# Kernel optimization log

Hardware: AMD Instinct MI355X
Metric: run time of the kernel (lower is better)

Reference implementation:

```python
import jax, jax.numpy as jnp
import numpy as np

N_NODES = 100000
N_EDGES = 600000
NFEAT = 128
HIDDEN = 64
NCLASS = 40


def _sage_conv(x, edge_index, Wl, bl, Wr):
    """PyG SAGEConv with mean aggregation.

    out = lin_l(mean_{j in N(i)} x_j) + lin_r(x_i)
    edge_index[0] = source j, edge_index[1] = target i.
    """
    src, dst = edge_index[0], edge_index[1]
    n = x.shape[0]
    # scatter-mean: sum messages then divide by in-degree (0-degree -> 0)
    msg_sum = jax.ops.segment_sum(x[src], dst, num_segments=n)          # [N, F]
    deg = jax.ops.segment_sum(jnp.ones_like(src, dtype=x.dtype), dst,
                              num_segments=n)                            # [N]
    agg = msg_sum / jnp.maximum(deg, 1.0)[:, None]
    return agg @ Wl + bl + x @ Wr


def setup_inputs() -> dict:
    key = jax.random.key(0)
    ks = jax.random.split(key, 8)
    x = jax.random.normal(ks[0], (N_NODES, NFEAT), dtype=jnp.float32)
    edge_index = jax.random.randint(ks[1], (2, N_EDGES), 0, N_NODES, dtype=jnp.int64)
    s1 = 1.0 / np.sqrt(NFEAT)
    s2 = 1.0 / np.sqrt(HIDDEN)
    return {
        "x": x,
        "edge_index": edge_index,
        "W1l": jax.random.uniform(ks[2], (NFEAT, HIDDEN), jnp.float32, -s1, s1),
        "b1": jnp.zeros((HIDDEN,), jnp.float32),
        "W1r": jax.random.uniform(ks[3], (NFEAT, HIDDEN), jnp.float32, -s1, s1),
        "W2l": jax.random.uniform(ks[4], (HIDDEN, NCLASS), jnp.float32, -s2, s2),
        "b2": jnp.zeros((NCLASS,), jnp.float32),
        "W2r": jax.random.uniform(ks[5], (HIDDEN, NCLASS), jnp.float32, -s2, s2),
    }


def reference(x, edge_index, W1l, b1, W1r, W2l, b2, W2r):
    h = _sage_conv(x, edge_index, W1l, b1, W1r)   # [N, 64]
    h = jax.nn.sigmoid(h)
    out = _sage_conv(h, edge_index, W2l, b2, W2r)  # [N, nclass]
    return out
```

## Files before the change

kernel.cpp:

```cpp
#include <hip/hip_runtime.h>
#include <hip/hip_bf16.h>


#define N_FEAT 128
#define HID 64
#define NCLS 40
#define NE_BLK 2048

typedef short short8 __attribute__((ext_vector_type(8)));
typedef float floatx4 __attribute__((ext_vector_type(4)));

static __device__ __forceinline__ short f2bf(float x) {
    __hip_bfloat16 h = __float2bfloat16(x);
    return __builtin_bit_cast(short, h);
}
static __device__ __forceinline__ float bf2f(unsigned short u) {
    unsigned int v = ((unsigned int)u) << 16;
    return __builtin_bit_cast(float, v);
}

__global__ void prep_hist(const float* __restrict__ W1l, const float* __restrict__ W1r,
                          const float* __restrict__ W2l, const float* __restrict__ W2r,
                          unsigned short* __restrict__ wt1,
                          unsigned short* __restrict__ wt2,
                          int* __restrict__ flags,
                          const int* __restrict__ ei, int ne, int n,
                          int* __restrict__ bh, int nbe) {
    __shared__ int bins[512];
    const int b = blockIdx.x, t = threadIdx.x;
    const int nbuck = (n + 255) >> 8;
    for (int i = t; i < nbuck; i += 256) bins[i] = 0;
    __syncthreads();
    const int e0 = b * NE_BLK;
    const int lim = (e0 + NE_BLK < ne) ? (e0 + NE_BLK) : ne;
    for (int e = e0 + t; e < lim; e += 256)
        atomicAdd(&bins[ei[ne + e] >> 8], 1);

    int i = b * 256 + t;
    if (i < 128 * 128) {
        int nn = i >> 7, k = i & 127;
        float v = (nn < 64) ? W1l[k * 64 + nn] : W1r[k * 64 + (nn - 64)];
        wt1[nn * 128 + k] = (unsigned short)f2bf(v);
    } else if (i < 128 * 128 + 48 * 128) {
        int j = i - 128 * 128;
        int nn = j >> 7, k = j & 127;
        float v = 0.f;
        if (nn < 40)
            v = (k < 64) ? W2l[k * 40 + nn] : W2r[(k - 64) * 40 + nn];
        wt2[nn * 128 + k] = (unsigned short)f2bf(v);
    }
    if (i < 256) flags[i] = 0;

    __syncthreads();
    for (int j = t; j < nbuck; j += 256) bh[j * nbe + b] = bins[j];
}

__global__ void scan_fused(const int* __restrict__ in, int* __restrict__ pre,
                           int m, int* __restrict__ bsums,
                           int* __restrict__ flags) {
    __shared__ int lds[256];
    __shared__ int look[128];
    __shared__ int sprefix;
    const int b = blockIdx.x, t = threadIdx.x;
    const int base = b * 2048 + t * 8;
    int v[8], s = 0;
#pragma unroll
    for (int i = 0; i < 8; ++i) {
        int idx = base + i;
        v[i] = (idx < m) ? in[idx] : 0;
        s += v[i];
    }
    lds[t] = s;
    __syncthreads();
    for (int o = 1; o < 256; o <<= 1) {
        int y = (t >= o) ? lds[t - o] : 0;
        __syncthreads();
        lds[t] += y;
        __syncthreads();
    }
    if (t == 255) {
        __hip_atomic_store(&bsums[b], lds[255], __ATOMIC_RELEASE,
                           __HIP_MEMORY_SCOPE_AGENT);
        __hip_atomic_store(&flags[b], 1, __ATOMIC_RELEASE,
                           __HIP_MEMORY_SCOPE_AGENT);
    }
    if (t < 128) look[t] = 0;
    __syncthreads();
    if (t < b) {
        while (__hip_atomic_load(&flags[t], __ATOMIC_ACQUIRE,
                                 __HIP_MEMORY_SCOPE_AGENT) == 0) {}
        look[t] = __hip_atomic_load(&bsums[t], __ATOMIC_RELAXED,
                                    __HIP_MEMORY_SCOPE_AGENT);
    }
    __syncthreads();
    if (t == 0) {
        int p = 0;
        for (int i = 0; i < b; ++i) p += look[i];
        sprefix = p;
    }
    __syncthreads();
    int run = ((t == 0) ? 0 : lds[t - 1]) + sprefix;
#pragma unroll
    for (int i = 0; i < 8; ++i) {
        run += v[i];
        int idx = base + i;
        if (idx < m) pre[idx + 1] = run;
    }
    if (b == 0 && t == 0) pre[0] = 0;
}

__global__ void bucket_scatter(const int* __restrict__ ei, int ne, int n,
                               const int* __restrict__ sbase,
                               int* __restrict__ ebuf, int nbe) {
    __shared__ int bins[512];
    const int b = blockIdx.x, t = threadIdx.x;
    const int nbuck = (n + 255) >> 8;
    for (int i = t; i < nbuck; i += 256) bins[i] = 0;
    __syncthreads();
    const int e0 = b * NE_BLK;
    const int lim = (e0 + NE_BLK < ne) ? (e0 + NE_BLK) : ne;
    for (int e = e0 + t; e < lim; e += 256) {
        int d = ei[ne + e];
        int s = ei[e];
        int bk = d >> 8;
        int r = atomicAdd(&bins[bk], 1);
        int p = sbase[bk * nbe + b] + r;
        ebuf[p] = (int)(((unsigned)(d & 255) << 24) | (unsigned)s);
    }
}

__global__ void bucket_build(const int* __restrict__ ebuf,
                             const int* __restrict__ sbase, int nbe, int n,
                             int ne, int* __restrict__ off,
                             int* __restrict__ csr) {
    __shared__ int cnt[256];
    __shared__ int sc[256];
    __shared__ int pos[256];
    const int b = blockIdx.x;
    const int t = threadIdx.x;
    const int nbuck = (n + 255) >> 8;
    const int s0 = sbase[b * nbe];
    const int s1 = (b + 1 < nbuck) ? sbase[(b + 1) * nbe] : ne;
    cnt[t] = 0;
    __syncthreads();
    for (int i = s0 + t; i < s1; i += 256)
        atomicAdd(&cnt[((unsigned)ebuf[i]) >> 24], 1);
    __syncthreads();
    int v = cnt[t];
    sc[t] = v;
    __syncthreads();
    for (int o = 1; o < 256; o <<= 1) {
        int y = (t >= o) ? sc[t - o] : 0;
        __syncthreads();
        sc[t] += y;
        __syncthreads();
    }
    int g = b * 256 + t;
    if (g < n) off[g + 1] = s0 + sc[t];
    if (b == 0 && t == 0) off[0] = 0;
    pos[t] = s0 + sc[t] - v;
    __syncthreads();
    for (int i = s0 + t; i < s1; i += 256) {
        unsigned w = (unsigned)ebuf[i];
        int p = atomicAdd(&pos[w >> 24], 1);
        csr[p] = (int)(w & 0xFFFFFFu);
    }
}

template <int K, int MH, bool AF32>
__global__ __launch_bounds__(256) void gemm_mfma(
    const void* __restrict__ Ain, const unsigned short* __restrict__ Wt,
    unsigned short* __restrict__ Zl, unsigned short* __restrict__ Zr, int n) {
    constexpr int M = 2 * MH;
    constexpr int LDA = K + 8;
    constexpr int MT = (M + 15) / 16;
    constexpr int KS = K / 32;
    constexpr int QROW = K / 8;
    __shared__ __align__(16) short At[64 * LDA];
    __shared__ __align__(16) short Bt[M * LDA];

    const int t = threadIdx.x;
    const int nodeBase = blockIdx.x * 64;

    for (int q = t; q < 64 * QROW; q += 256) {
        int row = q / QROW;
        int k0 = (q % QROW) * 8;
        int node = nodeBase + row;
        short8 s = {0, 0, 0, 0, 0, 0, 0, 0};
        if (node < n) {
            if (AF32) {
                const float* A = (const float*)Ain + (size_t)node * K + k0;
                float4 v0 = *(const float4*)A;
                float4 v1 = *(const float4*)(A + 4);
                s[0] = f2bf(v0.x); s[1] = f2bf(v0.y);
                s[2] = f2bf(v0.z); s[3] = f2bf(v0.w);
                s[4] = f2bf(v1.x); s[5] = f2bf(v1.y);
                s[6] = f2bf(v1.z); s[7] = f2bf(v1.w);
            } else {
                s = *(const short8*)((const short*)Ain + (size_t)node * K + k0);
            }
        }
        *(short8*)&At[row * LDA + k0] = s;
    }
    for (int q = t; q < M * QROW; q += 256) {
        int row = q / QROW;
        int k0 = (q % QROW) * 8;
        *(short8*)&Bt[row * LDA + k0] =
            *(const short8*)((const short*)Wt + (size_t)row * K + k0);
    }
    __syncthreads();

    const int wave = t >> 6;
    const int lane = t & 63;
    const int m0 = wave * 16;
    const int fl = lane & 15;
    const int quad = lane >> 4;

    floatx4 acc[MT];
#pragma unroll
    for (int nt = 0; nt < MT; ++nt) acc[nt] = (floatx4){0.f, 0.f, 0.f, 0.f};

#pragma unroll
    for (int ks = 0; ks < KS; ++ks) {
        const int kb = ks * 32 + quad * 8;
        short8 a = *(const short8*)&At[(m0 + fl) * LDA + kb];
#pragma unroll
        for (int nt = 0; nt < MT; ++nt) {
            short8 b = *(const short8*)&Bt[(nt * 16 + fl) * LDA + kb];
            acc[nt] = __builtin_amdgcn_mfma_f32_16x16x32_bf16(a, b, acc[nt], 0, 0, 0);
        }
    }

#pragma unroll
    for (int nt = 0; nt < MT; ++nt) {
        const int col = nt * 16 + fl;
#pragma unroll
        for (int r = 0; r < 4; ++r) {
            int node = nodeBase + m0 + quad * 4 + r;
            if (node < n) {
                unsigned short v = (unsigned short)f2bf(acc[nt][r]);
                if (col < MH)
                    Zl[(size_t)node * MH + col] = v;
                else
                    Zr[(size_t)node * MH + (col - MH)] = v;
            }
        }
    }
}

__global__ __launch_bounds__(256) void gemm2cat(
    const unsigned short* __restrict__ aggh, const unsigned short* __restrict__ h,
    const unsigned short* __restrict__ Wt, const float* __restrict__ bias,
    float* __restrict__ out, int n) {
    constexpr int K = 128;
    constexpr int LDA = K + 8;
    constexpr int M = 48;
    constexpr int MT = 3;
    __shared__ __align__(16) short At[64 * LDA];
    __shared__ __align__(16) short Bt[M * LDA];

    const int t = threadIdx.x;
    const int nodeBase = blockIdx.x * 64;

    for (int q = t; q < 64 * 16; q += 256) {
        int row = q >> 4;
        int k0 = (q & 15) * 8;
        int node = nodeBase + row;
        short8 s = {0, 0, 0, 0, 0, 0, 0, 0};
        if (node < n) {
            const unsigned short* src =
                (k0 < 64) ? (aggh + (size_t)node * 64 + k0)
                          : (h + (size_t)node * 64 + (k0 - 64));
            s = *(const short8*)src;
        }
        *(short8*)&At[row * LDA + k0] = s;
    }
    for (int q = t; q < M * 16; q += 256) {
        int row = q >> 4;
        int k0 = (q & 15) * 8;
        *(short8*)&Bt[row * LDA + k0] =
            *(const short8*)((const short*)Wt + (size_t)row * K + k0);
    }
    __syncthreads();

    const int wave = t >> 6;
    const int lane = t & 63;
    const int m0 = wave * 16;
    const int fl = lane & 15;
    const int quad = lane >> 4;

    floatx4 acc[MT];
#pragma unroll
    for (int nt = 0; nt < MT; ++nt) acc[nt] = (floatx4){0.f, 0.f, 0.f, 0.f};

#pragma unroll
    for (int ks = 0; ks < 4; ++ks) {
        const int kb = ks * 32 + quad * 8;
        short8 a = *(const short8*)&At[(m0 + fl) * LDA + kb];
#pragma unroll
        for (int nt = 0; nt < MT; ++nt) {
            short8 b = *(const short8*)&Bt[(nt * 16 + fl) * LDA + kb];
            acc[nt] = __builtin_amdgcn_mfma_f32_16x16x32_bf16(a, b, acc[nt], 0, 0, 0);
        }
    }

#pragma unroll
    for (int nt = 0; nt < MT; ++nt) {
        const int col = nt * 16 + fl;
        if (col < NCLS) {
            float bv = bias[col];
#pragma unroll
            for (int r = 0; r < 4; ++r) {
                int node = nodeBase + m0 + quad * 4 + r;
                if (node < n)
                    out[(size_t)node * NCLS + col] = acc[nt][r] + bv;
            }
        }
    }
}

template <int MODE>
__global__ void agg64_kernel(const unsigned short* __restrict__ Zl,
                             const unsigned short* __restrict__ Zr,
                             const int* __restrict__ off,
                             const int* __restrict__ csr,
                             const float* __restrict__ bias,
                             unsigned short* __restrict__ out, int n) {
    const int wid = blockIdx.x * (blockDim.x >> 6) + (threadIdx.x >> 6);
    const int node0 = wid * 2;
    if (node0 >= n) return;
    const int lane = threadIdx.x & 63;
    const int g = lane >> 3;
    const int c = lane & 7;

    const bool has1 = (node0 + 1) < n;
    const int s0 = off[node0];
    const int e0 = off[node0 + 1];
    const int e1 = has1 ? off[node0 + 2] : e0;
    const int d0 = e0 - s0;
    const int d1 = e1 - e0;

    int ed0 = (d0 > 0) ? csr[s0 + ((lane < d0) ? lane : (d0 - 1))] : 0;
    int ed1 = (d1 > 0) ? csr[e0 + ((lane < d1) ? lane : (d1 - 1))] : 0;

    float a0[8], a1[8];
#pragma unroll
    for (int j = 0; j < 8; ++j) { a0[j] = 0.f; a1[j] = 0.f; }

    const int dm = (d0 > d1) ? d0 : d1;
    for (int e = 0; e < dm; e += 8) {
        const int r = e + g;
        int i0, i1;
        if (e < 64) {
            i0 = __shfl(ed0, (r < d0) ? r : ((d0 > 0) ? d0 - 1 : 0));
            i1 = __shfl(ed1, (r < d1) ? r : ((d1 > 0) ? d1 - 1 : 0));
        } else {
            i0 = (d0 > 0) ? csr[s0 + ((r < d0) ? r : d0 - 1)] : 0;
            i1 = (d1 > 0) ? csr[e0 + ((r < d1) ? r : d1 - 1)] : 0;
        }
        const float w0 = (r < d0) ? 1.f : 0.f;
        const float w1 = (r < d1) ? 1.f : 0.f;
        uint4 v0 = *(const uint4*)(Zl + (size_t)i0 * 64 + c * 8);
        uint4 v1 = *(const uint4*)(Zl + (size_t)i1 * 64 + c * 8);
        a0[0] = fmaf(w0, bf2f((unsigned short)(v0.x & 0xffffu)), a0[0]);
        a0[1] = fmaf(w0, bf2f((unsigned short)(v0.x >> 16)), a0[1]);
        a0[2] = fmaf(w0, bf2f((unsigned short)(v0.y & 0xffffu)), a0[2]);
        a0[3] = fmaf(w0, bf2f((unsigned short)(v0.y >> 16)), a0[3]);
        a0[4] = fmaf(w0, bf2f((unsigned short)(v0.z & 0xffffu)), a0[4]);
        a0[5] = fmaf(w0, bf2f((unsigned short)(v0.z >> 16)), a0[5]);
        a0[6] = fmaf(w0, bf2f((unsigned short)(v0.w & 0xffffu)), a0[6]);
        a0[7] = fmaf(w0, bf2f((unsigned short)(v0.w >> 16)), a0[7]);
        a1[0] = fmaf(w1, bf2f((unsigned short)(v1.x & 0xffffu)), a1[0]);
        a1[1] = fmaf(w1, bf2f((unsigned short)(v1.x >> 16)), a1[1]);
        a1[2] = fmaf(w1, bf2f((unsigned short)(v1.y & 0xffffu)), a1[2]);
        a1[3] = fmaf(w1, bf2f((unsigned short)(v1.y >> 16)), a1[3]);
        a1[4] = fmaf(w1, bf2f((unsigned short)(v1.z & 0xffffu)), a1[4]);
        a1[5] = fmaf(w1, bf2f((unsigned short)(v1.z >> 16)), a1[5]);
        a1[6] = fmaf(w1, bf2f((unsigned short)(v1.w & 0xffffu)), a1[6]);
        a1[7] = fmaf(w1, bf2f((unsigned short)(v1.w >> 16)), a1[7]);
    }
#pragma unroll
    for (int o = 8; o < 64; o <<= 1) {
#pragma unroll
        for (int j = 0; j < 8; ++j) {
            a0[j] += __shfl_xor(a0[j], o);
            a1[j] += __shfl_xor(a1[j], o);
        }
    }
    if (g < 2) {
        const int node = node0 + g;
        if (node < n) {
            const int dd = g ? d1 : d0;
            float rr[8];
#pragma unroll
            for (int j = 0; j < 8; ++j) rr[j] = g ? a1[j] : a0[j];
            const float inv = 1.0f / fmaxf((float)dd, 1.0f);
            float r0, r1, r2, r3, r4, r5, r6, r7;
            if (MODE == 0) {
                uint4 z = *(const uint4*)(Zr + (size_t)node * 64 + c * 8);
                float4 b0 = ((const float4*)bias)[c * 2];
                float4 b1 = ((const float4*)bias)[c * 2 + 1];
                r0 = rr[0] * inv + bf2f((unsigned short)(z.x & 0xffffu)) + b0.x;
                r1 = rr[1] * inv + bf2f((unsigned short)(z.x >> 16)) + b0.y;
                r2 = rr[2] * inv + bf2f((unsigned short)(z.y & 0xffffu)) + b0.z;
                r3 = rr[3] * inv + bf2f((unsigned short)(z.y >> 16)) + b0.w;
                r4 = rr[4] * inv + bf2f((unsigned short)(z.z & 0xffffu)) + b1.x;
                r5 = rr[5] * inv + bf2f((unsigned short)(z.z >> 16)) + b1.y;
                r6 = rr[6] * inv + bf2f((unsigned short)(z.w & 0xffffu)) + b1.z;
                r7 = rr[7] * inv + bf2f((unsigned short)(z.w >> 16)) + b1.w;
                r0 = 1.0f / (1.0f + __expf(-r0));
                r1 = 1.0f / (1.0f + __expf(-r1));
                r2 = 1.0f / (1.0f + __expf(-r2));
                r3 = 1.0f / (1.0f + __expf(-r3));
                r4 = 1.0f / (1.0f + __expf(-r4));
                r5 = 1.0f / (1.0f + __expf(-r5));
                r6 = 1.0f / (1.0f + __expf(-r6));
                r7 = 1.0f / (1.0f + __expf(-r7));
            } else {
                r0 = rr[0] * inv; r1 = rr[1] * inv;
                r2 = rr[2] * inv; r3 = rr[3] * inv;
                r4 = rr[4] * inv; r5 = rr[5] * inv;
                r6 = rr[6] * inv; r7 = rr[7] * inv;
            }
            uint4 p;
            p.x = (unsigned int)(unsigned short)f2bf(r0) |
                  ((unsigned int)(unsigned short)f2bf(r1) << 16);
            p.y = (unsigned int)(unsigned short)f2bf(r2) |
                  ((unsigned int)(unsigned short)f2bf(r3) << 16);
            p.z = (unsigned int)(unsigned short)f2bf(r4) |
                  ((unsigned int)(unsigned short)f2bf(r5) << 16);
            p.w = (unsigned int)(unsigned short)f2bf(r6) |
                  ((unsigned int)(unsigned short)f2bf(r7) << 16);
            *(uint4*)(out + (size_t)node * 64 + c * 8) = p;
        }
    }
}

extern "C" void kernel_launch(void* const* d_in, const int* in_sizes, int n_in,
                              void* d_out, int out_size, void* d_ws,
                              size_t ws_size, hipStream_t stream) {
    const float* x = (const float*)d_in[0];
    const int* ei = (const int*)d_in[1];
    const float* W1l = (const float*)d_in[2];
    const float* b1 = (const float*)d_in[3];
    const float* W1r = (const float*)d_in[4];
    const float* W2l = (const float*)d_in[5];
    const float* b2 = (const float*)d_in[6];
    const float* W2r = (const float*)d_in[7];
    float* out = (float*)d_out;

    const int n = in_sizes[0] / N_FEAT;
    const int ne = in_sizes[1] / 2;

    const int nbe = (ne + NE_BLK - 1) / NE_BLK;
    const int nbuck = (n + 255) >> 8;
    const int tot = nbuck * nbe;

    unsigned short* zl1 = (unsigned short*)d_ws;
    unsigned short* zr1 = zl1 + (size_t)n * HID;
    unsigned short* h = zr1 + (size_t)n * HID;
    unsigned short* aggh = h + (size_t)n * HID;
    unsigned short* wt1 = aggh + (size_t)n * HID;
    unsigned short* wt2 = wt1 + 128 * 128;
    int* off = (int*)(wt2 + 48 * 128);
    int* csr = off + (n + 1);
    int* ebuf = csr + ne;
    int* bh = ebuf + ne;
    int* sbase = bh + tot;
    int* bsums = sbase + (tot + 1);
    int* flags = bsums + 256;

    const int gblocks = (n + 63) / 64;
    const int ablocks = (n + 7) / 8;
    const int nsb = (tot + 2047) / 2048;

    prep_hist<<<nbe, 256, 0, stream>>>(W1l, W1r, W2l, W2r, wt1, wt2, flags,
                                       ei, ne, n, bh, nbe);
    gemm_mfma<N_FEAT, HID, true><<<gblocks, 256, 0, stream>>>(x, wt1, zl1, zr1, n);
    scan_fused<<<nsb, 256, 0, stream>>>(bh, sbase, tot, bsums, flags);
    bucket_scatter<<<nbe, 256, 0, stream>>>(ei, ne, n, sbase, ebuf, nbe);
    bucket_build<<<nbuck, 256, 0, stream>>>(ebuf, sbase, nbe, n, ne, off, csr);
    agg64_kernel<0><<<ablocks, 256, 0, stream>>>(zl1, zr1, off, csr, b1, h, n);
    agg64_kernel<1><<<ablocks, 256, 0, stream>>>(h, nullptr, off, csr, nullptr,
                                                 aggh, n);
    gemm2cat<<<gblocks, 256, 0, stream>>>(aggh, h, wt2, b2, out, n);
}
```

Before: 218.0 us.

## Fuse layer-2 aggregation into GEMM2 and merge bucket scatter with GEMM1

Layer-2 mean aggregation now writes straight into the shared-memory A tile of the second GEMM, so the intermediate aggregated buffer and its global round trip are gone. The bucket scatter and the first GEMM run as one launch that splits work by block index, which removes a kernel launch and lets the two independent jobs overlap. Aggregation now processes 64 nodes per block and stages the block's CSR neighbour list in shared memory, falling back to global reads when it exceeds ECAP. In exchange the larger shared-memory footprint may lower occupancy, and blocks with very different node degrees may be unevenly loaded.

After: 216.6 us. Within noise of the previous version (-0.6%).

```diff
diff --git a/kernel.cpp b/kernel.cpp
--- a/kernel.cpp
+++ b/kernel.cpp
@@ -6,6 +6,7 @@
 #define HID 64
 #define NCLS 40
 #define NE_BLK 2048
+#define ECAP 1536
 
 typedef short short8 __attribute__((ext_vector_type(8)));
 typedef float floatx4 __attribute__((ext_vector_type(4)));
@@ -17,6 +18,16 @@
 static __device__ __forceinline__ float bf2f(unsigned short u) {
     unsigned int v = ((unsigned int)u) << 16;
     return __builtin_bit_cast(float, v);
+}
+static __device__ __forceinline__ void acc8(float* a, uint4 v, float w) {
+    a[0] = fmaf(w, bf2f((unsigned short)(v.x & 0xffffu)), a[0]);
+    a[1] = fmaf(w, bf2f((unsigned short)(v.x >> 16)), a[1]);
+    a[2] = fmaf(w, bf2f((unsigned short)(v.y & 0xffffu)), a[2]);
+    a[3] = fmaf(w, bf2f((unsigned short)(v.y >> 16)), a[3]);
+    a[4] = fmaf(w, bf2f((unsigned short)(v.z & 0xffffu)), a[4]);
+    a[5] = fmaf(w, bf2f((unsigned short)(v.z >> 16)), a[5]);
+    a[6] = fmaf(w, bf2f((unsigned short)(v.w & 0xffffu)), a[6]);
+    a[7] = fmaf(w, bf2f((unsigned short)(v.w >> 16)), a[7]);
 }
 
 __global__ void prep_hist(const float* __restrict__ W1l, const float* __restrict__ W1r,
@@ -109,23 +120,103 @@
     if (b == 0 && t == 0) pre[0] = 0;
 }
 
-__global__ void bucket_scatter(const int* __restrict__ ei, int ne, int n,
-                               const int* __restrict__ sbase,
-                               int* __restrict__ ebuf, int nbe) {
-    __shared__ int bins[512];
-    const int b = blockIdx.x, t = threadIdx.x;
-    const int nbuck = (n + 255) >> 8;
-    for (int i = t; i < nbuck; i += 256) bins[i] = 0;
-    __syncthreads();
-    const int e0 = b * NE_BLK;
-    const int lim = (e0 + NE_BLK < ne) ? (e0 + NE_BLK) : ne;
-    for (int e = e0 + t; e < lim; e += 256) {
-        int d = ei[ne + e];
-        int s = ei[e];
-        int bk = d >> 8;
-        int r = atomicAdd(&bins[bk], 1);
-        int p = sbase[bk * nbe + b] + r;
-        ebuf[p] = (int)(((unsigned)(d & 255) << 24) | (unsigned)s);
+static __device__ __forceinline__ void gemm1_body(
+    short* __restrict__ smem, const float* __restrict__ x,
+    const unsigned short* __restrict__ Wt, unsigned short* __restrict__ Zl,
+    unsigned short* __restrict__ Zr, int n, int bid) {
+    constexpr int K = 128, LDA = K + 8, M = 128, MT = 8, KS = 4, QROW = 16;
+    short* At = smem;
+    short* Bt = smem + 64 * LDA;
+    const int t = threadIdx.x;
+    const int nodeBase = bid * 64;
+
+    for (int q = t; q < 64 * QROW; q += 256) {
+        int row = q / QROW;
+        int k0 = (q % QROW) * 8;
+        int node = nodeBase + row;
+        short8 s = {0, 0, 0, 0, 0, 0, 0, 0};
+        if (node < n) {
+            const float* A = x + (size_t)node * K + k0;
+            float4 v0 = *(const float4*)A;
+            float4 v1 = *(const float4*)(A + 4);
+            s[0] = f2bf(v0.x); s[1] = f2bf(v0.y);
+            s[2] = f2bf(v0.z); s[3] = f2bf(v0.w);
+            s[4] = f2bf(v1.x); s[5] = f2bf(v1.y);
+            s[6] = f2bf(v1.z); s[7] = f2bf(v1.w);
+        }
+        *(short8*)&At[row * LDA + k0] = s;
+    }
+    for (int q = t; q < M * QROW; q += 256) {
+        int row = q / QROW;
+        int k0 = (q % QROW) * 8;
+        *(short8*)&Bt[row * LDA + k0] =
+            *(const short8*)((const short*)Wt + (size_t)row * K + k0);
+    }
+    __syncthreads();
+
+    const int wave = t >> 6;
+    const int lane = t & 63;
+    const int m0 = wave * 16;
+    const int fl = lane & 15;
+    const int quad = lane >> 4;
+
+    floatx4 acc[MT];
+#pragma unroll
+    for (int nt = 0; nt < MT; ++nt) acc[nt] = (floatx4){0.f, 0.f, 0.f, 0.f};
+
+#pragma unroll
+    for (int ks = 0; ks < KS; ++ks) {
+        const int kb = ks * 32 + quad * 8;
+        short8 a = *(const short8*)&At[(m0 + fl) * LDA + kb];
+#pragma unroll
+        for (int nt = 0; nt < MT; ++nt) {
+            short8 b = *(const short8*)&Bt[(nt * 16 + fl) * LDA + kb];
+            acc[nt] = __builtin_amdgcn_mfma_f32_16x16x32_bf16(a, b, acc[nt], 0, 0, 0);
+        }
+    }
+
+#pragma unroll
+    for (int nt = 0; nt < MT; ++nt) {
+        const int col = nt * 16 + fl;
+#pragma unroll
+        for (int r = 0; r < 4; ++r) {
+            int node = nodeBase + m0 + quad * 4 + r;
+            if (node < n) {
+                unsigned short v = (unsigned short)f2bf(acc[nt][r]);
+                if (col < HID)
+                    Zl[(size_t)node * HID + col] = v;
+                else
+                    Zr[(size_t)node * HID + (col - HID)] = v;
+            }
+        }
+    }
+}
+
+__global__ __launch_bounds__(256) void scatter_gemm1(
+    const int* __restrict__ ei, int ne, int n, const int* __restrict__ sbase,
+    int* __restrict__ ebuf, int nbe, const float* __restrict__ x,
+    const unsigned short* __restrict__ wt1, unsigned short* __restrict__ zl,
+    unsigned short* __restrict__ zr) {
+    __shared__ __align__(16) short smem[(64 + 128) * 136];
+    const int b = blockIdx.x;
+    if (b < nbe) {
+        int* bins = (int*)smem;
+        const int t = threadIdx.x;
+        const int nbuck = (n + 255) >> 8;
+        for (int i = t; i < nbuck; i += 256) bins[i] = 0;
+        __syncthreads();
+        const int e0 = b * NE_BLK;
+        const int lim = (e0 + NE_BLK < ne) ? (e0 + NE_BLK) : ne;
+        for (int e = e0 + t; e < lim; e += 256) {
+            int d = ei[ne + e];
+            int s = ei[e];
+            int bk = d >> 8;
+            int r = atomicAdd(&bins[bk], 1);
+            int p = sbase[bk * nbe + b] + r;
+            ebuf[p] = (int)(((unsigned)(d & 255) << 24) | (unsigned)s);
+        }
+    } else {
+        gemm1_body(smem, x, wt1, zl, zr, n, b - nbe);
     }
 }
 
@@ -167,271 +258,200 @@
     }
 }
 
-template <int K, int MH, bool AF32>
-__global__ __launch_bounds__(256) void gemm_mfma(
-    const void* __restrict__ Ain, const unsigned short* __restrict__ Wt,
-    unsigned short* __restrict__ Zl, unsigned short* __restrict__ Zr, int n) {
-    constexpr int M = 2 * MH;
-    constexpr int LDA = K + 8;
-    constexpr int MT = (M + 15) / 16;
-    constexpr int KS = K / 32;
-    constexpr int QROW = K / 8;
+__global__ __launch_bounds__(256) void agg_h(
+    const unsigned short* __restrict__ Zl, const unsigned short* __restrict__ Zr,
+    const int* __restrict__ off, const int* __restrict__ csr,
+    const float* __restrict__ bias, unsigned short* __restrict__ hout, int n) {
+    __shared__ int offs[65];
+    __shared__ int elist[ECAP];
+    const int t = threadIdx.x;
+    const int base = blockIdx.x * 64;
+    if (t < 65) {
+        int idx = base + t;
+        offs[t] = off[(idx <= n) ? idx : n];
+    }
+    __syncthreads();
+    const int E0 = offs[0];
+    const int nedge = offs[64] - E0;
+    const bool direct = (nedge > ECAP);
+    if (!direct)
+        for (int j = t; j < nedge; j += 256) elist[j] = csr[E0 + j];
+    __syncthreads();
+
+    const int lane = t & 63;
+    const int wave = t >> 6;
+    const int g = lane >> 3, c = lane & 7;
+
+    for (int p = 0; p < 8; ++p) {
+        const int i0 = wave * 16 + 2 * p, i1 = i0 + 1;
+        const int s0 = offs[i0] - E0, d0 = offs[i0 + 1] - offs[i0];
+        const int s1 = offs[i1] - E0, d1 = offs[i1 + 1] - offs[i1];
+        float a0[8], a1[8];
+#pragma unroll
+        for (int j = 0; j < 8; ++j) { a0[j] = 0.f; a1[j] = 0.f; }
+        const int dm = (d0 > d1) ? d0 : d1;
+        for (int r0 = 0; r0 < dm; r0 += 8) {
+            const int r = r0 + g;
+            int sl0 = s0 + ((r < d0) ? r : ((d0 > 0) ? d0 - 1 : 0));
+            int sl1 = s1 + ((r < d1) ? r : ((d1 > 0) ? d1 - 1 : 0));
+            int j0 = (d0 > 0) ? (direct ? csr[E0 + sl0] : elist[sl0]) : 0;
+            int j1 = (d1 > 0) ? (direct ? csr[E0 + sl1] : elist[sl1]) : 0;
+            uint4 v0 = *(const uint4*)(Zl + (size_t)j0 * 64 + c * 8);
+            uint4 v1 = *(const uint4*)(Zl + (size_t)j1 * 64 + c * 8);
+            acc8(a0, v0, (r < d0) ? 1.f : 0.f);
+            acc8(a1, v1, (r < d1) ? 1.f : 0.f);
+        }
+#pragma unroll
+        for (int o = 8; o < 64; o <<= 1) {
+#pragma unroll
+            for (int j = 0; j < 8; ++j) {
+                a0[j] += __shfl_xor(a0[j], o);
+                a1[j] += __shfl_xor(a1[j], o);
+            }
+        }
+        if (g < 2) {
+            const int i = g ? i1 : i0;
+            const int node = base + i;
+            if (node < n) {
+                const int dd = g ? d1 : d0;
+                const float inv = 1.0f / fmaxf((float)dd, 1.0f);
+                float rr[8];
+#pragma unroll
+                for (int j = 0; j < 8; ++j) rr[j] = (g ? a1[j] : a0[j]) * inv;
+                uint4 z = *(const uint4*)(Zr + (size_t)node * 64 + c * 8);
+                float4 b0 = ((const float4*)bias)[c * 2];
+                float4 b1 = ((const float4*)bias)[c * 2 + 1];
+                rr[0] += bf2f((unsigned short)(z.x & 0xffffu)) + b0.x;
+                rr[1] += bf2f((unsigned short)(z.x >> 16)) + b0.y;
+                rr[2] += bf2f((unsigned short)(z.y & 0xffffu)) + b0.z;
+                rr[3] += bf2f((unsigned short)(z.y >> 16)) + b0.w;
+                rr[4] += bf2f((unsigned short)(z.z & 0xffffu)) + b1.x;
+                rr[5] += bf2f((unsigned short)(z.z >> 16)) + b1.y;
+                rr[6] += bf2f((unsigned short)(z.w & 0xffffu)) + b1.z;
+                rr[7] += bf2f((unsigned short)(z.w >> 16)) + b1.w;
+#pragma unroll
+                for (int j = 0; j < 8; ++j)
+                    rr[j] = 1.0f / (1.0f + __expf(-rr[j]));
+                uint4 pk;
+                pk.x = (unsigned int)(unsigned short)f2bf(rr[0]) |
+                       ((unsigned int)(unsigned short)f2bf(rr[1]) << 16);
+                pk.y = (unsigned int)(unsigned short)f2bf(rr[2]) |
+                       ((unsigned int)(unsigned short)f2bf(rr[3]) << 16);
+                pk.z = (unsigned int)(unsigned short)f2bf(rr[4]) |
+                       ((unsigned int)(unsigned short)f2bf(rr[5]) << 16);
+                pk.w = (unsigned int)(unsigned short)f2bf(rr[6]) |
+                       ((unsigned int)(unsigned short)f2bf(rr[7]) << 16);
+                *(uint4*)(hout + (size_t)node * 64 + c * 8) = pk;
+            }
+        }
+    }
+}
+
+__global__ __launch_bounds__(256) void agg_gemm2(
+    const unsigned short* __restrict__ h, const unsigned short* __restrict__ Wt,
+    const float* __restrict__ bias, const int* __restrict__ off,
+    const int* __restrict__ csr, float* __restrict__ out, int n) {
+    constexpr int LDA = 136;
     __shared__ __align__(16) short At[64 * LDA];
-    __shared__ __align__(16) short Bt[M * LDA];
-
+    __shared__ __align__(16) short Bt[48 * LDA];
+    __shared__ int offs[65];
+    __shared__ int elist[ECAP];
     const int t = threadIdx.x;
-    const int nodeBase = blockIdx.x * 64;
-
-    for (int q = t; q < 64 * QROW; q += 256) {
-        int row = q / QROW;
-        int k0 = (q % QROW) * 8;
-        int node = nodeBase + row;
+    const int base = blockIdx.x * 64;
+    if (t < 65) {
+        int idx = base + t;
+        offs[t] = off[(idx <= n) ? idx : n];
+    }
+    __syncthreads();
+    const int E0 = offs[0];
+    const int nedge = offs[64] - E0;
+    const bool direct = (nedge > ECAP);
+    if (!direct)
+        for (int j = t; j < nedge; j += 256) elist[j] = csr[E0 + j];
+    for (int q = t; q < 64 * 8; q += 256) {
+        int row = q >> 3, k0 = (q & 7) * 8;
+        int node = base + row;
         short8 s = {0, 0, 0, 0, 0, 0, 0, 0};
-        if (node < n) {
-            if (AF32) {
-                const float* A = (const float*)Ain + (size_t)node * K + k0;
-                float4 v0 = *(const float4*)A;
-                float4 v1 = *(const float4*)(A + 4);
-                s[0] = f2bf(v0.x); s[1] = f2bf(v0.y);
-                s[2] = f2bf(v0.z); s[3] = f2bf(v0.w);
-                s[4] = f2bf(v1.x); s[5] = f2bf(v1.y);
-                s[6] = f2bf(v1.z); s[7] = f2bf(v1.w);
-            } else {
-                s = *(const short8*)((const short*)Ain + (size_t)node * K + k0);
+        if (node < n) s = *(const short8*)(h + (size_t)node * 64 + k0);
+        *(short8*)&At[row * LDA + 64 + k0] = s;
+    }
+    for (int q = t; q < 48 * 16; q += 256) {
+        int row = q >> 4, k0 = (q & 15) * 8;
+        *(short8*)&Bt[row * LDA + k0] =
+            *(const short8*)((const short*)Wt + (size_t)row * 128 + k0);
+    }
+    __syncthreads();
+
+    const int lane = t & 63;
+    const int wave = t >> 6;
+    const int g = lane >> 3, c = lane & 7;
+    for (int p = 0; p < 8; ++p) {
+        const int i0 = wave * 16 + 2 * p, i1 = i0 + 1;
+        const int s0 = offs[i0] - E0, d0 = offs[i0 + 1] - offs[i0];
+        const int s1 = offs[i1] - E0, d1 = offs[i1 + 1] - offs[i1];
+        float a0[8], a1[8];
+#pragma unroll
+        for (int j = 0; j < 8; ++j) { a0[j] = 0.f; a1[j] = 0.f; }
+        const int dm = (d0 > d1) ? d0 : d1;
+        for (int r0 = 0; r0 < dm; r0 += 8) {
+            const int r = r0 + g;
+            int sl0 = s0 + ((r < d0) ? r : ((d0 > 0) ? d0 - 1 : 0));
+            int sl1 = s1 + ((r < d1) ? r : ((d1 > 0) ? d1 - 1 : 0));
+            int j0 = (d0 > 0) ? (direct ? csr[E0 + sl0] : elist[sl0]) : 0;
+            int j1 = (d1 > 0) ? (direct ? csr[E0 + sl1] : elist[sl1]) : 0;
+            uint4 v0 = *(const uint4*)(h + (size_t)j0 * 64 + c * 8);
+            uint4 v1 = *(const uint4*)(h + (size_t)j1 * 64 + c * 8);
+            acc8(a0, v0, (r < d0) ? 1.f : 0.f);
+            acc8(a1, v1, (r < d1) ? 1.f : 0.f);
+        }
+#pragma unroll
+        for (int o = 8; o < 64; o <<= 1) {
+#pragma unroll
+            for (int j = 0; j < 8; ++j) {
+                a0[j] += __shfl_xor(a0[j], o);
+                a1[j] += __shfl_xor(a1[j], o);
             }
         }
-        *(short8*)&At[row * LDA + k0] = s;
-    }
-    for (int q = t; q < M * QROW; q += 256) {
-        int row = q / QROW;
-        int k0 = (q % QROW) * 8;
-        *(short8*)&Bt[row * LDA + k0] =
-            *(const short8*)((const short*)Wt + (size_t)row * K + k0);
-    }
-    __syncthreads();
-
-    const int wave = t >> 6;
-    const int lane = t & 63;
+        if (g < 2) {
+            const int i = g ? i1 : i0;
+            const int dd = g ? d1 : d0;
+            const float inv = 1.0f / fmaxf((float)dd, 1.0f);
+            short8 s;
+#pragma unroll
+            for (int j = 0; j < 8; ++j)
+                s[j] = f2bf((g ? a1[j] : a0[j]) * inv);
+            *(short8*)&At[i * LDA + c * 8] = s;
+        }
+    }
+    __syncthreads();
+
     const int m0 = wave * 16;
     const int fl = lane & 15;
     const int quad = lane >> 4;
-
-    floatx4 acc[MT];
-#pragma unroll
-    for (int nt = 0; nt < MT; ++nt) acc[nt] = (floatx4){0.f, 0.f, 0.f, 0.f};
-
-#pragma unroll
-    for (int ks = 0; ks < KS; ++ks) {
-        const int kb = ks * 32 + quad * 8;
-        short8 a = *(const short8*)&At[(m0 + fl) * LDA + kb];
-#pragma unroll
-        for (int nt = 0; nt < MT; ++nt) {
-            short8 b = *(const short8*)&Bt[(nt * 16 + fl) * LDA + kb];
-            acc[nt] = __builtin_amdgcn_mfma_f32_16x16x32_bf16(a, b, acc[nt], 0, 0, 0);
-        }
-    }
-
-#pragma unroll
-    for (int nt = 0; nt < MT; ++nt) {
-        const int col = nt * 16 + fl;
-#pragma unroll
-        for (int r = 0; r < 4; ++r) {
-            int node = nodeBase + m0 + quad * 4 + r;
-            if (node < n) {
-                unsigned short v = (unsigned short)f2bf(acc[nt][r]);
-                if (col < MH)
-                    Zl[(size_t)node * MH + col] = v;
-                else
-                    Zr[(size_t)node * MH + (col - MH)] = v;
-            }
-        }
-    }
-}
-
-__global__ __launch_bounds__(256) void gemm2cat(
-    const unsigned short* __restrict__ aggh, const unsigned short* __restrict__ h,
-    const unsigned short* __restrict__ Wt, const float* __restrict__ bias,
-    float* __restrict__ out, int n) {
-    constexpr int K = 128;
-    constexpr int LDA = K + 8;
-    constexpr int M = 48;
-    constexpr int MT = 3;
-    __shared__ __align__(16) short At[64 * LDA];
-    __shared__ __align__(16) short Bt[M * LDA];
-
-    const int t = threadIdx.x;
-    const int nodeBase = blockIdx.x * 64;
-
-    for (int q = t; q < 64 * 16; q += 256) {
-        int row = q >> 4;
-        int k0 = (q & 15) * 8;
-        int node = nodeBase + row;
-        short8 s = {0, 0, 0, 0, 0, 0, 0, 0};
-        if (node < n) {
-            const unsigned short* src =
-                (k0 < 64) ? (aggh + (size_t)node * 64 + k0)
-                          : (h + (size_t)node * 64 + (k0 - 64));
-            s = *(const short8*)src;
-        }
-        *(short8*)&At[row * LDA + k0] = s;
-    }
-    for (int q = t; q < M * 16; q += 256) {
-        int row = q >> 4;
-        int k0 = (q & 15) * 8;
-        *(short8*)&Bt[row * LDA + k0] =
-            *(const short8*)((const short*)Wt + (size_t)row * K + k0);
-    }
-    __syncthreads();
-
-    const int wave = t >> 6;
-    const int lane = t & 63;
-    const int m0 = wave * 16;
-    const int fl = lane & 15;
-    const int quad = lane >> 4;
-
-    floatx4 acc[MT];
-#pragma unroll
-    for (int nt = 0; nt < MT; ++nt) acc[nt] = (floatx4){0.f, 0.f, 0.f, 0.f};
-
+    floatx4 acc[3];
+#pragma unroll
+    for (int nt = 0; nt < 3; ++nt) acc[nt] = (floatx4){0.f, 0.f, 0.f, 0.f};
 #pragma unroll
     for (int ks = 0; ks < 4; ++ks) {
         const int kb = ks * 32 + quad * 8;
         short8 a = *(const short8*)&At[(m0 + fl) * LDA + kb];
 #pragma unroll
-        for (int nt = 0; nt < MT; ++nt) {
+        for (int nt = 0; nt < 3; ++nt) {
             short8 b = *(const short8*)&Bt[(nt * 16 + fl) * LDA + kb];
             acc[nt] = __builtin_amdgcn_mfma_f32_16x16x32_bf16(a, b, acc[nt], 0, 0, 0);
         }
     }
-
-#pragma unroll
-    for (int nt = 0; nt < MT; ++nt) {
+#pragma unroll
+    for (int nt = 0; nt < 3; ++nt) {
         const int col = nt * 16 + fl;
         if (col < NCLS) {
             float bv = bias[col];
 #pragma unroll
             for (int r = 0; r < 4; ++r) {
-                int node = nodeBase + m0 + quad * 4 + r;
+                int node = base + m0 + quad * 4 + r;
                 if (node < n)
                     out[(size_t)node * NCLS + col] = acc[nt][r] + bv;
             }
-        }
-    }
-}
-
-template <int MODE>
-__global__ void agg64_kernel(const unsigned short* __restrict__ Zl,
-                             const unsigned short* __restrict__ Zr,
-                             const int* __restrict__ off,
-                             const int* __restrict__ csr,
-                             const float* __restrict__ bias,
-                             unsigned short* __restrict__ out, int n) {
-    const int wid = blockIdx.x * (blockDim.x >> 6) + (threadIdx.x >> 6);
-    const int node0 = wid * 2;
-    if (node0 >= n) return;
-    const int lane = threadIdx.x & 63;
-    const int g = lane >> 3;
-    const int c = lane & 7;
-
-    const bool has1 = (node0 + 1) < n;
-    const int s0 = off[node0];
-    const int e0 = off[node0 + 1];
-    const int e1 = has1 ? off[node0 + 2] : e0;
-    const int d0 = e0 - s0;
-    const int d1 = e1 - e0;
-
-    int ed0 = (d0 > 0) ? csr[s0 + ((lane < d0) ? lane : (d0 - 1))] : 0;
-    int ed1 = (d1 > 0) ? csr[e0 + ((lane < d1) ? lane : (d1 - 1))] : 0;
-
-    float a0[8], a1[8];
-#pragma unroll
-    for (int j = 0; j < 8; ++j) { a0[j] = 0.f; a1[j] = 0.f; }
-
-    const int dm = (d0 > d1) ? d0 : d1;
-    for (int e = 0; e < dm; e += 8) {
-        const int r = e + g;
-        int i0, i1;
-        if (e < 64) {
-            i0 = __shfl(ed0, (r < d0) ? r : ((d0 > 0) ? d0 - 1 : 0));
-            i1 = __shfl(ed1, (r < d1) ? r : ((d1 > 0) ? d1 - 1 : 0));
-        } else {
-            i0 = (d0 > 0) ? csr[s0 + ((r < d0) ? r : d0 - 1)] : 0;
-            i1 = (d1 > 0) ? csr[e0 + ((r < d1) ? r : d1 - 1)] : 0;
-        }
-        const float w0 = (r < d0) ? 1.f : 0.f;
-        const float w1 = (r < d1) ? 1.f : 0.f;
-        uint4 v0 = *(const uint4*)(Zl + (size_t)i0 * 64 + c * 8);
-        uint4 v1 = *(const uint4*)(Zl + (size_t)i1 * 64 + c * 8);
-        a0[0] = fmaf(w0, bf2f((unsigned short)(v0.x & 0xffffu)), a0[0]);
-        a0[1] = fmaf(w0, bf2f((unsigned short)(v0.x >> 16)), a0[1]);
-        a0[2] = fmaf(w0, bf2f((unsigned short)(v0.y & 0xffffu)), a0[2]);
-        a0[3] = fmaf(w0, bf2f((unsigned short)(v0.y >> 16)), a0[3]);
-        a0[4] = fmaf(w0, bf2f((unsigned short)(v0.z & 0xffffu)), a0[4]);
-        a0[5] = fmaf(w0, bf2f((unsigned short)(v0.z >> 16)), a0[5]);
-        a0[6] = fmaf(w0, bf2f((unsigned short)(v0.w & 0xffffu)), a0[6]);
-        a0[7] = fmaf(w0, bf2f((unsigned short)(v0.w >> 16)), a0[7]);
-        a1[0] = fmaf(w1, bf2f((unsigned short)(v1.x & 0xffffu)), a1[0]);
-        a1[1] = fmaf(w1, bf2f((unsigned short)(v1.x >> 16)), a1[1]);
-        a1[2] = fmaf(w1, bf2f((unsigned short)(v1.y & 0xffffu)), a1[2]);
-        a1[3] = fmaf(w1, bf2f((unsigned short)(v1.y >> 16)), a1[3]);
-        a1[4] = fmaf(w1, bf2f((unsigned short)(v1.z & 0xffffu)), a1[4]);
-        a1[5] = fmaf(w1, bf2f((unsigned short)(v1.z >> 16)), a1[5]);
-        a1[6] = fmaf(w1, bf2f((unsigned short)(v1.w & 0xffffu)), a1[6]);
-        a1[7] = fmaf(w1, bf2f((unsigned short)(v1.w >> 16)), a1[7]);
-    }
-#pragma unroll
-    for (int o = 8; o < 64; o <<= 1) {
-#pragma unroll
-        for (int j = 0; j < 8; ++j) {
-            a0[j] += __shfl_xor(a0[j], o);
-            a1[j] += __shfl_xor(a1[j], o);
-        }
-    }
-    if (g < 2) {
-        const int node = node0 + g;
-        if (node < n) {
-            const int dd = g ? d1 : d0;
-            float rr[8];
-#pragma unroll
-            for (int j = 0; j < 8; ++j) rr[j] = g ? a1[j] : a0[j];
-            const float inv = 1.0f / fmaxf((float)dd, 1.0f);
-            float r0, r1, r2, r3, r4, r5, r6, r7;
-            if (MODE == 0) {
-                uint4 z = *(const uint4*)(Zr + (size_t)node * 64 + c * 8);
-                float4 b0 = ((const float4*)bias)[c * 2];
-                float4 b1 = ((const float4*)bias)[c * 2 + 1];
-                r0 = rr[0] * inv + bf2f((unsigned short)(z.x & 0xffffu)) + b0.x;
-                r1 = rr[1] * inv + bf2f((unsigned short)(z.x >> 16)) + b0.y;
-                r2 = rr[2] * inv + bf2f((unsigned short)(z.y & 0xffffu)) + b0.z;
-                r3 = rr[3] * inv + bf2f((unsigned short)(z.y >> 16)) + b0.w;
-                r4 = rr[4] * inv + bf2f((unsigned short)(z.z & 0xffffu)) + b1.x;
-                r5 = rr[5] * inv + bf2f((unsigned short)(z.z >> 16)) + b1.y;
-                r6 = rr[6] * inv + bf2f((unsigned short)(z.w & 0xffffu)) + b1.z;
-                r7 = rr[7] * inv + bf2f((unsigned short)(z.w >> 16)) + b1.w;
-                r0 = 1.0f / (1.0f + __expf(-r0));
-                r1 = 1.0f / (1.0f + __expf(-r1));
-                r2 = 1.0f / (1.0f + __expf(-r2));
-                r3 = 1.0f / (1.0f + __expf(-r3));
-                r4 = 1.0f / (1.0f + __expf(-r4));
-                r5 = 1.0f / (1.0f + __expf(-r5));
-                r6 = 1.0f / (1.0f + __expf(-r6));
-                r7 = 1.0f / (1.0f + __expf(-r7));
-            } else {
-                r0 = rr[0] * inv; r1 = rr[1] * inv;
-                r2 = rr[2] * inv; r3 = rr[3] * inv;
-                r4 = rr[4] * inv; r5 = rr[5] * inv;
-                r6 = rr[6] * inv; r7 = rr[7] * inv;
-            }
-            uint4 p;
-            p.x = (unsigned int)(unsigned short)f2bf(r0) |
-                  ((unsigned int)(unsigned short)f2bf(r1) << 16);
-            p.y = (unsigned int)(unsigned short)f2bf(r2) |
-                  ((unsigned int)(unsigned short)f2bf(r3) << 16);
-            p.z = (unsigned int)(unsigned short)f2bf(r4) |
-                  ((unsigned int)(unsigned short)f2bf(r5) << 16);
-            p.w = (unsigned int)(unsigned short)f2bf(r6) |
-                  ((unsigned int)(unsigned short)f2bf(r7) << 16);
-            *(uint4*)(out + (size_t)node * 64 + c * 8) = p;
         }
     }
 }
@@ -459,8 +479,7 @@
     unsigned short* zl1 = (unsigned short*)d_ws;
     unsigned short* zr1 = zl1 + (size_t)n * HID;
     unsigned short* h = zr1 + (size_t)n * HID;
-    unsigned short* aggh = h + (size_t)n * HID;
-    unsigned short* wt1 = aggh + (size_t)n * HID;
+    unsigned short* wt1 = h + (size_t)n * HID;
     unsigned short* wt2 = wt1 + 128 * 128;
     int* off = (int*)(wt2 + 48 * 128);
     int* csr = off + (n + 1);
@@ -471,17 +490,14 @@
     int* flags = bsums + 256;
 
     const int gblocks = (n + 63) / 64;
-    const int ablocks = (n + 7) / 8;
     const int nsb = (tot + 2047) / 2048;
 
     prep_hist<<<nbe, 256, 0, stream>>>(W1l, W1r, W2l, W2r, wt1, wt2, flags,
                                        ei, ne, n, bh, nbe);
-    gemm_mfma<N_FEAT, HID, true><<<gblocks, 256, 0, stream>>>(x, wt1, zl1, zr1, n);
     scan_fused<<<nsb, 256, 0, stream>>>(bh, sbase, tot, bsums, flags);
-    bucket_scatter<<<nbe, 256, 0, stream>>>(ei, ne, n, sbase, ebuf, nbe);
+    scatter_gemm1<<<nbe + gblocks, 256, 0, stream>>>(ei, ne, n, sbase, ebuf,
+                                                     nbe, x, wt1, zl1, zr1);
     bucket_build<<<nbuck, 256, 0, stream>>>(ebuf, sbase, nbe, n, ne, off, csr);
-    agg64_kernel<0><<<ablocks, 256, 0, stream>>>(zl1, zr1, off, csr, b1, h, n);
-    agg64_kernel<1><<<ablocks, 256, 0, stream>>>(h, nullptr, off, csr, nullptr,
-                                                 aggh, n);
-    gemm2cat<<<gblocks, 256, 0, stream>>>(aggh, h, wt2, b2, out, n);
-}
+    agg_h<<<gblocks, 256, 0, stream>>>(zl1, zr1, off, csr, b1, h, n);
+    agg_gemm2<<<gblocks, 256, 0, stream>>>(h, wt2, b2, off, csr, out, n);
+}
```
